# Kernel optimization log

Hardware: AMD Instinct MI355X
Metric: run time of the kernel (lower is better)

The kernel has to match this reference:

```python
import jax, jax.numpy as jnp
import numpy as np

# Module hyperparameters (from init_kwargs)
THRESHOLD = 1.0
TAU_MEM = 20.0
TAU_ADP = 200.0
BETA = 0.1          # adaptive-threshold coupling
SG_BETA = 10.0      # fast_sigmoid surrogate slope
ALPHA_MEM = float(np.exp(-1.0 / TAU_MEM))
ALPHA_ADP = float(np.exp(-1.0 / TAU_ADP))


@jax.custom_vjp
def spike_fn(u):
    # SpikingFunction.forward: (input >= threshold).float()
    return (u >= THRESHOLD).astype(u.dtype)

def _spike_fwd(u):
    return spike_fn(u), u

def _spike_bwd(u, g):
    # fast_sigmoid surrogate on (input - threshold)
    return (g / (1.0 + jnp.abs(SG_BETA * (u - THRESHOLD))),)

spike_fn.defvjp(_spike_fwd, _spike_bwd)


def setup_inputs() -> dict:
    key = jax.random.key(0)
    x = jax.random.normal(key, (32, 512, 1024), dtype=jnp.float32)  # [B, T, D]
    return {"x": x}


def reference(x):
    B = x.shape[0]
    state_shape = (B,) + x.shape[2:]
    v0 = jnp.zeros(state_shape, dtype=x.dtype)  # membrane potential
    a0 = jnp.zeros(state_shape, dtype=x.dtype)  # adaptive threshold

    def step(carry, x_t):
        v, a = carry
        v = ALPHA_MEM * v + x_t
        cur_thr = THRESHOLD + BETA * a
        # NOTE: original passes (v - cur_thr) into a spike fn that itself
        # compares against THRESHOLD, so the threshold counts twice.
        s = spike_fn(v - cur_thr)
        a = ALPHA_ADP * a + s
        v = v - s * THRESHOLD  # reset == 'subtract'
        return (v, a), s

    x_tmajor = jnp.swapaxes(x, 0, 1)  # [T, B, D]
    _, spikes = jax.lax.scan(step, (v0, a0), x_tmajor)
    return jnp.swapaxes(spikes, 0, 1)  # [B, T, D]
```

## Files before the change

### kernel.cpp

```cpp
#include <hip/hip_runtime.h>


#define T_STEPS 512
#define D_DIM   1024

#define ALPHA_MEM 0.9512294245007141f
#define ALPHA_ADP 0.9950124791926823f

__device__ __forceinline__ float adlif_step(float xv, float& v, float& a) {
    v = __fadd_rn(__fmul_rn(ALPHA_MEM, v), xv);
    float cur = __fadd_rn(1.0f, __fmul_rn(0.1f, a));
    float u = __fsub_rn(v, cur);
    float s = (u >= 1.0f) ? 1.0f : 0.0f;
    a = __fadd_rn(__fmul_rn(ALPHA_ADP, a), s);
    v = __fsub_rn(v, s);
    return s;
}

__global__ __launch_bounds__(64) void adlif_kernel(const float* __restrict__ x,
                                                   float* __restrict__ out) {
    const int idx = blockIdx.x * 64 + threadIdx.x;
    const int b = idx >> 10;
    const int d = idx & (D_DIM - 1);
    const size_t base = (size_t)b * (T_STEPS * D_DIM) + d;
    const float* xp = x + base;
    float* op = out + base;

    float v = 0.0f, a = 0.0f;

    constexpr int L = 64;
    float buf[L];

#pragma unroll
    for (int i = 0; i < L; ++i) buf[i] = xp[i * D_DIM];

    for (int t0 = 0; t0 < T_STEPS - L; t0 += L) {
#pragma unroll
        for (int i = 0; i < L; ++i) {
            float nx = xp[(t0 + L + i) * D_DIM];
            float s = adlif_step(buf[i], v, a);
            __builtin_nontemporal_store(s, &op[(t0 + i) * D_DIM]);
            buf[i] = nx;
        }
    }

#pragma unroll
    for (int i = 0; i < L; ++i) {
        float s = adlif_step(buf[i], v, a);
        __builtin_nontemporal_store(s, &op[(T_STEPS - L + i) * D_DIM]);
    }
}

extern "C" void kernel_launch(void* const* d_in, const int* in_sizes, int n_in,
                              void* d_out, int out_size, void* d_ws, size_t ws_size,
                              hipStream_t stream) {
    const float* x = (const float*)d_in[0];
    float* out = (float*)d_out;

    const int total = in_sizes[0];
    const int channels = total / T_STEPS;
    const int blocks = channels / 64;

    adlif_kernel<<<blocks, 64, 0, stream>>>(x, out);
}
```

Measured before the change: 31.16 us.

## Warp-specialize ADLIF scan with LDS-staged loads and bit-packed spike stores

```diff
diff --git a/kernel.cpp b/kernel.cpp
--- a/kernel.cpp
+++ b/kernel.cpp
@@ -3,51 +3,103 @@
 
 #define T_STEPS 512
 #define D_DIM   1024
+#define T_TILE  64
+#define N_TILES (T_STEPS / T_TILE)
+#define LDS_PITCH 68
 
 #define ALPHA_MEM 0.9512294245007141f
 #define ALPHA_ADP 0.9950124791926823f
 
-__device__ __forceinline__ float adlif_step(float xv, float& v, float& a) {
+typedef float f32x4 __attribute__((ext_vector_type(4)));
+
+__device__ __forceinline__ bool adlif_step(float xv, float& v, float& a) {
     v = __fadd_rn(__fmul_rn(ALPHA_MEM, v), xv);
     float cur = __fadd_rn(1.0f, __fmul_rn(0.1f, a));
     float u = __fsub_rn(v, cur);
-    float s = (u >= 1.0f) ? 1.0f : 0.0f;
+    bool fired = (u >= 1.0f);
+    float s = fired ? 1.0f : 0.0f;
     a = __fadd_rn(__fmul_rn(ALPHA_ADP, a), s);
     v = __fsub_rn(v, s);
-    return s;
+    return fired;
 }
 
-__global__ __launch_bounds__(64) void adlif_kernel(const float* __restrict__ x,
+__device__ __forceinline__ void load_tile(const float* __restrict__ xb, int t0,
+                                          int lane, float (*buf)[LDS_PITCH]) {
+    const int r0 = lane >> 4;
+    const int m  = lane & 15;
+    const float* src = xb + (size_t)(t0 + r0) * D_DIM + m * 4;
+    f32x4 v[16];
+#pragma unroll
+    for (int i = 0; i < 16; ++i)
+        v[i] = *reinterpret_cast<const f32x4*>(src + (size_t)i * 4 * D_DIM);
+#pragma unroll
+    for (int i = 0; i < 16; ++i)
+        *reinterpret_cast<f32x4*>(&buf[i * 4 + r0][m * 4]) = v[i];
+}
+
+__global__ __launch_bounds__(512) void adlif_fused(const float* __restrict__ x,
                                                    float* __restrict__ out) {
-    const int idx = blockIdx.x * 64 + threadIdx.x;
-    const int b = idx >> 10;
-    const int d = idx & (D_DIM - 1);
-    const size_t base = (size_t)b * (T_STEPS * D_DIM) + d;
-    const float* xp = x + base;
-    float* op = out + base;
+    __shared__ float    tiles[4][T_TILE][LDS_PITCH];
+    __shared__ unsigned sbits[2][64][2];
+
+    const int lane = threadIdx.x & 63;
+    const int wave = threadIdx.x >> 6;
+    const int bid  = blockIdx.x;
+    const int b    = bid >> 4;
+    const int dgrp = bid & 15;
+    const float* xb = x   + (size_t)b * (T_STEPS * D_DIM) + dgrp * 64;
+    float*       ob = out + (size_t)b * (T_STEPS * D_DIM) + dgrp * 64;
+
+    if (wave >= 1 && wave <= 3)
+        load_tile(xb, (wave - 1) * T_TILE, lane, tiles[wave - 1]);
+    __syncthreads();
 
     float v = 0.0f, a = 0.0f;
 
-    constexpr int L = 64;
-    float buf[L];
-
+    for (int k = 0; k <= N_TILES; ++k) {
+        if (wave == 0) {
+            if (k < N_TILES) {
+                unsigned wlo = 0u, whi = 0u;
 #pragma unroll
-    for (int i = 0; i < L; ++i) buf[i] = xp[i * D_DIM];
-
-    for (int t0 = 0; t0 < T_STEPS - L; t0 += L) {
+                for (int j = 0; j < T_TILE; ++j) {
+                    const float xv = tiles[k & 3][j][lane];
+                    const bool f = adlif_step(xv, v, a);
+                    if (j < 32) wlo |= ((unsigned)f) << j;
+                    else        whi |= ((unsigned)f) << (j - 32);
+                }
+                sbits[k & 1][lane][0] = wlo;
+                sbits[k & 1][lane][1] = whi;
+            }
+        } else if (wave <= 3) {
+            const int t = k + 3;
+            if (t < N_TILES && wave == (t % 3) + 1)
+                load_tile(xb, t * T_TILE, lane, tiles[t & 3]);
+        } else {
+            if (k >= 1) {
+                const int kt = k - 1;
+                const int r0 = (wave - 4) * 16;
+                const int c0 = (lane & 15) * 4;
+                const int rl = lane >> 4;
+                const int half = (r0 >= 32) ? 1 : 0;
+                const unsigned w0 = sbits[kt & 1][c0 + 0][half];
+                const unsigned w1 = sbits[kt & 1][c0 + 1][half];
+                const unsigned w2 = sbits[kt & 1][c0 + 2][half];
+                const unsigned w3 = sbits[kt & 1][c0 + 3][half];
 #pragma unroll
-        for (int i = 0; i < L; ++i) {
-            float nx = xp[(t0 + L + i) * D_DIM];
-            float s = adlif_step(buf[i], v, a);
-            __builtin_nontemporal_store(s, &op[(t0 + i) * D_DIM]);
-            buf[i] = nx;
+                for (int i = 0; i < 4; ++i) {
+                    const int r = r0 + i * 4 + rl;
+                    const int bitpos = r & 31;
+                    f32x4 val;
+                    val.x = (float)((w0 >> bitpos) & 1u);
+                    val.y = (float)((w1 >> bitpos) & 1u);
+                    val.z = (float)((w2 >> bitpos) & 1u);
+                    val.w = (float)((w3 >> bitpos) & 1u);
+                    __builtin_nontemporal_store(
+                        val, (f32x4*)(ob + (size_t)(kt * T_TILE + r) * D_DIM + c0));
+                }
+            }
         }
-    }
-
-#pragma unroll
-    for (int i = 0; i < L; ++i) {
-        float s = adlif_step(buf[i], v, a);
-        __builtin_nontemporal_store(s, &op[(T_STEPS - L + i) * D_DIM]);
+        __syncthreads();
     }
 }
 
@@ -61,5 +113,5 @@
     const int channels = total / T_STEPS;
     const int blocks = channels / 64;
 
-    adlif_kernel<<<blocks, 64, 0, stream>>>(x, out);
+    adlif_fused<<<blocks, 512, 0, stream>>>(x, out);
 }
```

Measured after the change: 27.44 us. 11.9% less time.
